# Kernel tuning notes

Hardware: AMD Instinct MI355X
Metric: run time of the kernel (lower is better)

The kernel has to match this reference:

```python
import jax, jax.numpy as jnp
import numpy as np

H = 96          # hidden_dim / GatedGraphConv out_channels
L = 6           # num_layers
F_IN = 32       # num_node_features
G = 4096        # number of graphs in batch
BN_EPS = 1e-5


def setup_inputs() -> dict:
    key = jax.random.key(0)
    ks = jax.random.split(key, 16)
    N, E = 100000, 400000
    x = jax.random.normal(ks[0], (N, F_IN), dtype=jnp.float32)
    edge_index = jax.random.randint(ks[1], (2, E), 0, N, dtype=jnp.int64)
    batch = jnp.sort(jax.random.randint(ks[2], (N,), 0, G, dtype=jnp.int64))
    s = 1.0 / np.sqrt(H)
    conv_w = jax.random.uniform(ks[3], (L, H, H), jnp.float32, -s, s)
    w_ih = jax.random.uniform(ks[4], (3 * H, H), jnp.float32, -s, s)
    w_hh = jax.random.uniform(ks[5], (3 * H, H), jnp.float32, -s, s)
    b_ih = jax.random.uniform(ks[6], (3 * H,), jnp.float32, -s, s)
    b_hh = jax.random.uniform(ks[7], (3 * H,), jnp.float32, -s, s)
    bn_gamma = jnp.ones((H,), jnp.float32)
    bn_beta = jnp.zeros((H,), jnp.float32)
    s1 = 1.0 / np.sqrt(H)
    fc1_w = jax.random.uniform(ks[8], (4 * H, H), jnp.float32, -s1, s1)
    fc1_b = jax.random.uniform(ks[9], (4 * H,), jnp.float32, -s1, s1)
    s2 = 1.0 / np.sqrt(4 * H)
    fc2_w = jax.random.uniform(ks[10], (H, 4 * H), jnp.float32, -s2, s2)
    fc2_b = jax.random.uniform(ks[11], (H,), jnp.float32, -s2, s2)
    fc3_w = jax.random.uniform(ks[12], (1, H), jnp.float32, -s1, s1)
    fc3_b = jax.random.uniform(ks[13], (1,), jnp.float32, -s1, s1)
    return dict(x=x, edge_index=edge_index, batch=batch, conv_w=conv_w,
                w_ih=w_ih, w_hh=w_hh, b_ih=b_ih, b_hh=b_hh,
                bn_gamma=bn_gamma, bn_beta=bn_beta,
                fc1_w=fc1_w, fc1_b=fc1_b, fc2_w=fc2_w, fc2_b=fc2_b,
                fc3_w=fc3_w, fc3_b=fc3_b)


def _gated_graph_conv(x, src, dst, conv_w, w_ih, w_hh, b_ih, b_hh):
    N = x.shape[0]
    # PyG zero-pads input features up to out_channels
    h = jnp.pad(x, ((0, 0), (0, H - x.shape[1])))
    for i in range(L):
        m = h @ conv_w[i]                         # [N, H]
        agg = jnp.zeros((N, H), m.dtype).at[dst].add(m[src])  # scatter-add at targets
        gi = agg @ w_ih.T + b_ih                  # [N, 3H]
        gh = h @ w_hh.T + b_hh                    # [N, 3H]
        i_r, i_z, i_n = jnp.split(gi, 3, axis=-1)
        h_r, h_z, h_n = jnp.split(gh, 3, axis=-1)
        r = jax.nn.sigmoid(i_r + h_r)
        z = jax.nn.sigmoid(i_z + h_z)
        n = jnp.tanh(i_n + r * h_n)
        h = (1.0 - z) * n + z * h
    return h


def reference(x, edge_index, batch, conv_w, w_ih, w_hh, b_ih, b_hh,
              bn_gamma, bn_beta, fc1_w, fc1_b, fc2_w, fc2_b, fc3_w, fc3_b):
    src, dst = edge_index[0], edge_index[1]
    h = _gated_graph_conv(x, src, dst, conv_w, w_ih, w_hh, b_ih, b_hh)
    h = jax.nn.relu(h)
    # global mean pool (dropout is identity in eval)
    sums = jax.ops.segment_sum(h, batch, num_segments=G)          # [G, H]
    counts = jax.ops.segment_sum(jnp.ones((h.shape[0],), h.dtype), batch, num_segments=G)
    pooled = sums / jnp.maximum(counts, 1.0)[:, None]
    # BatchNorm1d in eval mode: running_mean=0, running_var=1
    hbn = (pooled / jnp.sqrt(1.0 + BN_EPS)) * bn_gamma + bn_beta
    h1 = jax.nn.relu(hbn @ fc1_w.T + fc1_b)
    h2 = jax.nn.relu(h1 @ fc2_w.T + fc2_b)
    return h2 @ fc3_w.T + fc3_b                                    # [G, 1]
```

## Files before the change

kernel.cpp:

```cpp
#include <hip/hip_runtime.h>

#define H96 96
#define LAYERS 6
#define BN_EPS 1e-5f
#define SCAN_B 1024

typedef unsigned short u16;
typedef unsigned int u32;
typedef _Float16 f16;
typedef _Float16 h8 __attribute__((ext_vector_type(8)));
typedef float f32x4 __attribute__((ext_vector_type(4)));
typedef float f32x2 __attribute__((ext_vector_type(2)));
typedef u32 u32x3 __attribute__((ext_vector_type(3)));

__device__ __forceinline__ float sigm(float x) { return 1.f / (1.f + __expf(-x)); }
__device__ __forceinline__ float tanh_(float x) { return 2.f / (1.f + __expf(-2.f * x)) - 1.f; }
__device__ __forceinline__ f32x4 splat4(float x) { f32x4 v = {x, x, x, x}; return v; }
__device__ __forceinline__ h8 H8(f32x4 v) { return __builtin_bit_cast(h8, v); }

struct h2s { f16 x, y; };

__device__ __forceinline__ void upk(u32 v, float& lo, float& hi) {
    union { u32 u; h2s h; } c;
    c.u = v;
    lo = (float)c.h.x;
    hi = (float)c.h.y;
}

__device__ __forceinline__ h8 lds_frag(const f16* p) {
    union { h8 v; f32x2 h[2]; } u;
    u.h[0] = *(const f32x2*)(p);
    u.h[1] = *(const f32x2*)(p + 4);
    return u.v;
}

__global__ void k_f2h(const float* __restrict__ convw, const float* __restrict__ wih,
                      const float* __restrict__ whh, const float* __restrict__ fc1w,
                      const float* __restrict__ fc2w, f16* __restrict__ dst) {
    int i = blockIdx.x * 256 + threadIdx.x;
    if (i >= 184320) return;
    float v;
    if (i < 55296) v = convw[i];
    else if (i < 82944) v = wih[i - 55296];
    else if (i < 110592) v = whh[i - 82944];
    else if (i < 147456) v = fc1w[i - 110592];
    else v = fc2w[i - 147456];
    dst[i] = (f16)v;
}

__global__ __launch_bounds__(256) void k_wpt(const f16* __restrict__ wih16, const f16* __restrict__ convw16,
                                             f16* __restrict__ wpt) {
    int l = blockIdx.y;
    int lane = threadIdx.x & 63, wave = threadIdx.x >> 6;
    int l15 = lane & 15, q = lane >> 4;
    int rowa = blockIdx.x * 64 + wave * 16 + l15;
    if (rowa >= 288) rowa = 287;
    const f16* B = convw16 + (size_t)l * 9216;
    h8 af[3];
#pragma unroll
    for (int s = 0; s < 3; s++) af[s] = *(const h8*)(wih16 + (size_t)rowa * 96 + s * 32 + q * 8);
    f32x4 acc[6];
#pragma unroll
    for (int t = 0; t < 6; t++) acc[t] = splat4(0.f);
#pragma unroll
    for (int s = 0; s < 3; s++)
#pragma unroll
        for (int t = 0; t < 6; t++) {
            h8 b = *(const h8*)(B + (size_t)(t * 16 + l15) * 96 + s * 32 + q * 8);
            acc[t] = __builtin_amdgcn_mfma_f32_16x16x32_f16(af[s], b, acc[t], 0, 0, 0);
        }
    int rbase = blockIdx.x * 64 + wave * 16 + q * 4;
#pragma unroll
    for (int t = 0; t < 6; t++)
#pragma unroll
        for (int rr = 0; rr < 4; rr++) {
            int row = rbase + rr;
            if (row < 288) wpt[(size_t)l * 27648 + (size_t)row * 96 + t * 16 + l15] = (f16)acc[t][rr];
        }
}

__global__ void k_pad(const float* __restrict__ x, f16* __restrict__ hf, int N) {
    int i = blockIdx.x * 256 + threadIdx.x;
    if (i >= N * H96) return;
    int n = i / H96, c = i - n * H96;
    float v = (c < 32) ? x[n * 32 + c] : 0.f;
    hf[i] = (f16)v;
}

__global__ void k_hist(const int* __restrict__ key, int* __restrict__ deg, int E) {
    int e = blockIdx.x * 256 + threadIdx.x;
    if (e < E) atomicAdd(&deg[key[e]], 1);
}

__global__ __launch_bounds__(SCAN_B) void k_scan1(const int* __restrict__ deg, int* __restrict__ incl,
                                                  int* __restrict__ bsum, int N) {
    __shared__ int sh[SCAN_B];
    int i = blockIdx.x * SCAN_B + threadIdx.x;
    int v = (i < N) ? deg[i] : 0;
    sh[threadIdx.x] = v;
    __syncthreads();
    for (int off = 1; off < SCAN_B; off <<= 1) {
        int t = (threadIdx.x >= (u32)off) ? sh[threadIdx.x - off] : 0;
        __syncthreads();
        sh[threadIdx.x] += t;
        __syncthreads();
    }
    incl[blockIdx.x * SCAN_B + threadIdx.x] = sh[threadIdx.x];
    if (threadIdx.x == SCAN_B - 1) bsum[blockIdx.x] = sh[threadIdx.x];
}

__global__ void k_scan2(int* __restrict__ bsum, int nb) {
    if (blockIdx.x == 0 && threadIdx.x == 0) {
        int run = 0;
        for (int i = 0; i < nb; i++) { run += bsum[i]; bsum[i] = run; }
    }
}

__global__ void k_scan3(const int* __restrict__ deg, const int* __restrict__ incl, const int* __restrict__ bsum,
                        int* __restrict__ rs, int* __restrict__ cur, int N, int E) {
    int i = blockIdx.x * 256 + threadIdx.x;
    if (i == 0) rs[N] = E;
    if (i < N) {
        int b = i / SCAN_B;
        int off = (b > 0) ? bsum[b - 1] : 0;
        int ex = incl[i] - deg[i] + off;
        rs[i] = ex;
        if (cur) cur[i] = ex;
    }
}

__global__ void k_fill(const int* __restrict__ src, const int* __restrict__ dst, int* __restrict__ cur,
                       int* __restrict__ es, int E) {
    int e = blockIdx.x * 256 + threadIdx.x;
    if (e < E) {
        int p = atomicAdd(&cur[dst[e]], 1);
        es[p] = src[e];
    }
}

__global__ __launch_bounds__(256) void k_gather(const f16* __restrict__ hin, const int* __restrict__ rs,
                                                const int* __restrict__ es, f16* __restrict__ agg, int N) {
    int grp = threadIdx.x >> 4;
    int lane6 = threadIdx.x & 15;
    int node = blockIdx.x * 16 + grp;
    if (node >= N) return;
    int s = rs[node], e = rs[node + 1];
    float a0 = 0, a1 = 0, a2 = 0, a3 = 0, a4 = 0, a5 = 0;
    const char* basep = (const char*)hin;
    int off = lane6 * 12;
    for (int i = s; i < e; i += 4) {
        int j1 = (i + 1 < e) ? i + 1 : i;
        int j2 = (i + 2 < e) ? i + 2 : i;
        int j3 = (i + 3 < e) ? i + 3 : i;
        float m1 = (i + 1 < e) ? 1.f : 0.f;
        float m2 = (i + 2 < e) ? 1.f : 0.f;
        float m3 = (i + 3 < e) ? 1.f : 0.f;
        int sa = es[i], sb = es[j1], sc = es[j2], sd = es[j3];
        u32x3 va = *(const u32x3*)(basep + (size_t)sa * 192 + off);
        u32x3 vb = *(const u32x3*)(basep + (size_t)sb * 192 + off);
        u32x3 vc = *(const u32x3*)(basep + (size_t)sc * 192 + off);
        u32x3 vd = *(const u32x3*)(basep + (size_t)sd * 192 + off);
        float t0, t1;
        upk(va.x, t0, t1); a0 += t0; a1 += t1;
        upk(va.y, t0, t1); a2 += t0; a3 += t1;
        upk(va.z, t0, t1); a4 += t0; a5 += t1;
        upk(vb.x, t0, t1); a0 += t0 * m1; a1 += t1 * m1;
        upk(vb.y, t0, t1); a2 += t0 * m1; a3 += t1 * m1;
        upk(vb.z, t0, t1); a4 += t0 * m1; a5 += t1 * m1;
        upk(vc.x, t0, t1); a0 += t0 * m2; a1 += t1 * m2;
        upk(vc.y, t0, t1); a2 += t0 * m2; a3 += t1 * m2;
        upk(vc.z, t0, t1); a4 += t0 * m2; a5 += t1 * m2;
        upk(vd.x, t0, t1); a0 += t0 * m3; a1 += t1 * m3;
        upk(vd.y, t0, t1); a2 += t0 * m3; a3 += t1 * m3;
        upk(vd.z, t0, t1); a4 += t0 * m3; a5 += t1 * m3;
    }
    f16* dp = agg + (size_t)node * H96 + lane6 * 6;
    h2s p0, p1, p2;
    p0.x = (f16)a0; p0.y = (f16)a1;
    p1.x = (f16)a2; p1.y = (f16)a3;
    p2.x = (f16)a4; p2.y = (f16)a5;
    *(h2s*)(dp + 0) = p0;
    *(h2s*)(dp + 2) = p1;
    *(h2s*)(dp + 4) = p2;
}

__global__ __launch_bounds__(384, 2) void k_gru(const f16* __restrict__ agg, const f16* __restrict__ hin,
                                                f16* __restrict__ hout, const f16* __restrict__ wpt,
                                                const f16* __restrict__ whh, const float* __restrict__ bih,
                                                const float* __restrict__ bhh, int N) {
    const int TP = 100;
    __shared__ f16 sA[2][16 * TP];
    __shared__ f16 sH[2][16 * TP];
    int tid = threadIdx.x;
    int w = tid >> 6;
    int lane = tid & 63;
    int l15 = lane & 15, q = lane >> 4;
    int jr = w * 16 + l15;
    float b_r = bih[jr] + bhh[jr];
    float b_z = bih[96 + jr] + bhh[96 + jr];
    float b_in = bih[192 + jr];
    float b_hn = bhh[192 + jr];
    f32x4 wr0[3], wr1[3], wz0[3], wz1[3], wn0[3], wn1[3];
#pragma unroll
    for (int s = 0; s < 3; s++) {
        int ko = s * 32 + q * 8;
        wr0[s] = *(const f32x4*)(wpt + (size_t)jr * H96 + ko);
        wz0[s] = *(const f32x4*)(wpt + (size_t)(96 + jr) * H96 + ko);
        wn0[s] = *(const f32x4*)(wpt + (size_t)(192 + jr) * H96 + ko);
        wr1[s] = *(const f32x4*)(whh + (size_t)jr * H96 + ko);
        wz1[s] = *(const f32x4*)(whh + (size_t)(96 + jr) * H96 + ko);
        wn1[s] = *(const f32x4*)(whh + (size_t)(192 + jr) * H96 + ko);
    }
#pragma unroll
    for (int s = 0; s < 3; s++) {
        asm volatile("" : "+v"(wr0[s]), "+v"(wr1[s]), "+v"(wz0[s]), "+v"(wz1[s]), "+v"(wn0[s]), "+v"(wn1[s]));
    }

    int mt = (tid < 192) ? tid : tid - 192;
    int mrow = mt / 12;
    int mcol = mt - mrow * 12;
    const f16* smat = (tid < 192) ? agg : hin;
    f16* sdst = (tid < 192) ? &sA[0][0] : &sH[0][0];
    int soff = mrow * TP + mcol * 8;

    int ntiles = (N + 15) >> 4;
    int stride = gridDim.x;
    int tile = blockIdx.x;
    if (tile >= ntiles) return;

    {
        int rowa = (tile << 4) + mrow;
        if (rowa >= N) rowa = N - 1;
        f32x4 v = *(const f32x4*)(smat + (size_t)rowa * 96 + mcol * 8);
        union { f32x4 v; f32x2 h[2]; } u;
        u.v = v;
        *(f32x2*)(sdst + soff) = u.h[0];
        *(f32x2*)(sdst + soff + 4) = u.h[1];
    }
    __syncthreads();
    int cur = 0;
    while (true) {
        int nxt = tile + stride;
        bool havenext = nxt < ntiles;
        f32x4 v2 = splat4(0.f);
        if (havenext) {
            int rowa = (nxt << 4) + mrow;
            if (rowa >= N) rowa = N - 1;
            v2 = *(const f32x4*)(smat + (size_t)rowa * 96 + mcol * 8);
        }
        const f16* pA = &sA[cur][0];
        const f16* pH = &sH[cur][0];
        h8 as_[3], ah[3];
#pragma unroll
        for (int s = 0; s < 3; s++) {
            int off = l15 * TP + s * 32 + q * 8;
            as_[s] = lds_frag(pA + off);
            ah[s] = lds_frag(pH + off);
        }
        f32x4 r = splat4(b_r), z = splat4(b_z), nn = splat4(b_in), hn = splat4(b_hn);
#pragma unroll
        for (int s = 0; s < 3; s++) {
            r = __builtin_amdgcn_mfma_f32_16x16x32_f16(as_[s], H8(wr0[s]), r, 0, 0, 0);
            r = __builtin_amdgcn_mfma_f32_16x16x32_f16(ah[s], H8(wr1[s]), r, 0, 0, 0);
            z = __builtin_amdgcn_mfma_f32_16x16x32_f16(as_[s], H8(wz0[s]), z, 0, 0, 0);
            z = __builtin_amdgcn_mfma_f32_16x16x32_f16(ah[s], H8(wz1[s]), z, 0, 0, 0);
            nn = __builtin_amdgcn_mfma_f32_16x16x32_f16(as_[s], H8(wn0[s]), nn, 0, 0, 0);
            hn = __builtin_amdgcn_mfma_f32_16x16x32_f16(ah[s], H8(wn1[s]), hn, 0, 0, 0);
        }
        int base = tile << 4;
        int rbase = base + q * 4;
#pragma unroll
        for (int rr = 0; rr < 4; rr++) {
            int row = rbase + rr;
            if (row < N) {
                float rv = sigm(r[rr]);
                float zv = sigm(z[rr]);
                float nv = tanh_(nn[rr] + rv * hn[rr]);
                float hold = (float)pH[(q * 4 + rr) * TP + w * 16 + l15];
                float hnew = (1.f - zv) * nv + zv * hold;
                hout[(size_t)row * H96 + w * 16 + l15] = (f16)hnew;
            }
        }
        __syncthreads();
        if (!havenext) break;
        {
            union { f32x4 v; f32x2 h[2]; } u;
            u.v = v2;
            f16* d2 = sdst + (cur ^ 1) * (16 * TP) + soff;
            *(f32x2*)(d2) = u.h[0];
            *(f32x2*)(d2 + 4) = u.h[1];
        }
        __syncthreads();
        tile = nxt;
        cur ^= 1;
    }
}

__global__ void k_pool2(const f16* __restrict__ hf, const int* __restrict__ grs,
                        const float* __restrict__ gamma, const float* __restrict__ beta,
                        f16* __restrict__ pooled, int Gn) {
    int g = blockIdx.x;
    int c = threadIdx.x;
    if (g >= Gn || c >= H96) return;
    int s = grs[g], e = grs[g + 1];
    float sum = 0.f;
    for (int n = s; n < e; n++) sum += fmaxf((float)hf[(size_t)n * H96 + c], 0.f);
    float cnt = fmaxf((float)(e - s), 1.f);
    float val = (sum / cnt) * (gamma[c] * rsqrtf(1.f + BN_EPS)) + beta[c];
    pooled[(size_t)g * H96 + c] = (f16)val;
}

template <int KS, int NT, int OUTW, bool RELU>
__global__ __launch_bounds__(256) void k_mlp(const f16* __restrict__ A, const f16* __restrict__ W,
                                             const float* __restrict__ bias, f16* __restrict__ out, int M) {
    int lane = threadIdx.x & 63, wave = threadIdx.x >> 6;
    int l15 = lane & 15, q = lane >> 4;
    int colBase = blockIdx.y * (NT * 16);
    int tile = blockIdx.x;
    int rowa = tile * 64 + wave * 16 + l15;
    if (rowa >= M) rowa = M - 1;
    h8 af[KS];
#pragma unroll
    for (int s = 0; s < KS; s++) af[s] = *(const h8*)(A + (size_t)rowa * (KS * 32) + s * 32 + q * 8);
    f32x4 acc[NT];
#pragma unroll
    for (int t = 0; t < NT; t++) acc[t] = splat4(0.f);
#pragma unroll
    for (int s = 0; s < KS; s++)
#pragma unroll
        for (int t = 0; t < NT; t++) {
            h8 b = *(const h8*)(W + (size_t)(colBase + t * 16 + l15) * (KS * 32) + s * 32 + q * 8);
            acc[t] = __builtin_amdgcn_mfma_f32_16x16x32_f16(af[s], b, acc[t], 0, 0, 0);
        }
    int rbase = tile * 64 + wave * 16 + q * 4;
#pragma unroll
    for (int t = 0; t < NT; t++) {
        float bv = bias[colBase + t * 16 + l15];
#pragma unroll
        for (int rr = 0; rr < 4; rr++) {
            int row = rbase + rr;
            if (row >= M) continue;
            float v = acc[t][rr] + bv;
            if (RELU) v = fmaxf(v, 0.f);
            out[(size_t)row * OUTW + colBase + t * 16 + l15] = (f16)v;
        }
    }
}

__global__ void k_mlp3(const f16* __restrict__ h2, const float* __restrict__ w, const float* __restrict__ b,
                       float* __restrict__ out, int M) {
    int g = blockIdx.x * 256 + threadIdx.x;
    if (g >= M) return;
    float acc = 0.f;
    for (int k = 0; k < H96; k++) acc += (float)h2[(size_t)g * H96 + k] * w[k];
    out[g] = acc + b[0];
}

extern "C" void kernel_launch(void* const* d_in, const int* in_sizes, int n_in, void* d_out, int out_size,
                              void* d_ws, size_t ws_size, hipStream_t stream) {
    const float* x = (const float*)d_in[0];
    const int* ei = (const int*)d_in[1];
    const int* batch = (const int*)d_in[2];
    const float* conv_w = (const float*)d_in[3];
    const float* wih = (const float*)d_in[4];
    const float* whh = (const float*)d_in[5];
    const float* bih = (const float*)d_in[6];
    const float* bhh = (const float*)d_in[7];
    const float* gamma = (const float*)d_in[8];
    const float* beta = (const float*)d_in[9];
    const float* fc1w = (const float*)d_in[10];
    const float* fc1b = (const float*)d_in[11];
    const float* fc2w = (const float*)d_in[12];
    const float* fc2b = (const float*)d_in[13];
    const float* fc3w = (const float*)d_in[14];
    const float* fc3b = (const float*)d_in[15];

    int N = in_sizes[0] / 32;
    int E = in_sizes[1] / 2;
    int Gn = out_size;
    const int* srcp = ei;
    const int* dstp = ei + E;

    char* p = (char*)d_ws;
    auto alloc = [&](size_t bytes) -> char* {
        char* r = p;
        p += (bytes + 255) & ~(size_t)255;
        return r;
    };
    f16* hA = (f16*)alloc((size_t)N * H96 * 2);
    f16* hB = (f16*)alloc((size_t)N * H96 * 2);
    f16* aggf = (f16*)alloc((size_t)N * H96 * 2);
    f16* wf16 = (f16*)alloc((size_t)184320 * 2);
    f16* wpt = (f16*)alloc((size_t)LAYERS * 27648 * 2);
    int nb = (N + SCAN_B - 1) / SCAN_B;
    int* deg = (int*)alloc((size_t)N * 4);
    int* incl = (int*)alloc((size_t)nb * SCAN_B * 4);
    int* bsum = (int*)alloc((size_t)nb * 4);
    int* rs = (int*)alloc((size_t)(N + 1) * 4);
    int* cur = (int*)alloc((size_t)N * 4);
    int* es = (int*)alloc((size_t)E * 4);
    int nb2 = (Gn + SCAN_B - 1) / SCAN_B;
    int* gdeg = (int*)alloc((size_t)Gn * 4);
    int* gincl = (int*)alloc((size_t)nb2 * SCAN_B * 4);
    int* gbsum = (int*)alloc((size_t)nb2 * 4);
    int* grs = (int*)alloc((size_t)(Gn + 1) * 4);
    f16* pooled = (f16*)alloc((size_t)Gn * H96 * 2);
    f16* h1 = (f16*)alloc((size_t)Gn * 384 * 2);
    f16* h2 = (f16*)alloc((size_t)Gn * H96 * 2);

    f16* convw16 = wf16;
    f16* wih16 = wf16 + 55296;
    f16* whh16 = wf16 + 82944;
    f16* fc1w16 = wf16 + 110592;
    f16* fc2w16 = wf16 + 147456;

    hipMemsetAsync(deg, 0, (size_t)N * 4, stream);
    hipMemsetAsync(gdeg, 0, (size_t)Gn * 4, stream);

    k_f2h<<<720, 256, 0, stream>>>(conv_w, wih, whh, fc1w, fc2w, wf16);
    k_wpt<<<dim3(5, 6), 256, 0, stream>>>(wih16, convw16, wpt);
    k_pad<<<(N * H96 + 255) / 256, 256, 0, stream>>>(x, hA, N);
    k_hist<<<(E + 255) / 256, 256, 0, stream>>>(dstp, deg, E);
    k_scan1<<<nb, SCAN_B, 0, stream>>>(deg, incl, bsum, N);
    k_scan2<<<1, 64, 0, stream>>>(bsum, nb);
    k_scan3<<<(N + 255) / 256, 256, 0, stream>>>(deg, incl, bsum, rs, cur, N, E);
    k_fill<<<(E + 255) / 256, 256, 0, stream>>>(srcp, dstp, cur, es, E);
    k_hist<<<(N + 255) / 256, 256, 0, stream>>>(batch, gdeg, N);
    k_scan1<<<nb2, SCAN_B, 0, stream>>>(gdeg, gincl, gbsum, Gn);
    k_scan2<<<1, 64, 0, stream>>>(gbsum, nb2);
    k_scan3<<<(Gn + 255) / 256, 256, 0, stream>>>(gdeg, gincl, gbsum, grs, (int*)nullptr, Gn, N);

    int nt16 = (N + 15) / 16;
    for (int l = 0; l < LAYERS; l++) {
        f16* hin = (l & 1) ? hB : hA;
        f16* hout = (l & 1) ? hA : hB;
        k_gather<<<nt16, 256, 0, stream>>>(hin, rs, es, aggf, N);
        k_gru<<<1280, 384, 0, stream>>>(aggf, hin, hout, wpt + (size_t)l * 27648, whh16, bih, bhh, N);
    }

    k_pool2<<<Gn, 128, 0, stream>>>(hA, grs, gamma, beta, pooled, Gn);
    k_mlp<3, 6, 384, true><<<dim3((Gn + 63) / 64, 4), 256, 0, stream>>>(pooled, fc1w16, fc1b, h1, Gn);
    k_mlp<12, 6, 96, true><<<dim3((Gn + 63) / 64, 1), 256, 0, stream>>>(h1, fc2w16, fc2b, h2, Gn);
    k_mlp3<<<(Gn + 255) / 256, 256, 0, stream>>>(h2, fc3w, fc3b, (float*)d_out, Gn);
}
```

Baseline: 610.4 us.

## Fuse neighbor gather into GRU layer kernel, aggregating into shared memory

Measured after the change: 743.4 us. 1.22x slower.

```diff
diff --git a/kernel.cpp b/kernel.cpp
--- a/kernel.cpp
+++ b/kernel.cpp
@@ -11,7 +11,7 @@
 typedef _Float16 h8 __attribute__((ext_vector_type(8)));
 typedef float f32x4 __attribute__((ext_vector_type(4)));
 typedef float f32x2 __attribute__((ext_vector_type(2)));
-typedef u32 u32x3 __attribute__((ext_vector_type(3)));
+typedef u32 u32x2 __attribute__((ext_vector_type(2)));
 
 __device__ __forceinline__ float sigm(float x) { return 1.f / (1.f + __expf(-x)); }
 __device__ __forceinline__ float tanh_(float x) { return 2.f / (1.f + __expf(-2.f * x)) - 1.f; }
@@ -138,59 +138,14 @@
     }
 }
 
-__global__ __launch_bounds__(256) void k_gather(const f16* __restrict__ hin, const int* __restrict__ rs,
-                                                const int* __restrict__ es, f16* __restrict__ agg, int N) {
-    int grp = threadIdx.x >> 4;
-    int lane6 = threadIdx.x & 15;
-    int node = blockIdx.x * 16 + grp;
-    if (node >= N) return;
-    int s = rs[node], e = rs[node + 1];
-    float a0 = 0, a1 = 0, a2 = 0, a3 = 0, a4 = 0, a5 = 0;
-    const char* basep = (const char*)hin;
-    int off = lane6 * 12;
-    for (int i = s; i < e; i += 4) {
-        int j1 = (i + 1 < e) ? i + 1 : i;
-        int j2 = (i + 2 < e) ? i + 2 : i;
-        int j3 = (i + 3 < e) ? i + 3 : i;
-        float m1 = (i + 1 < e) ? 1.f : 0.f;
-        float m2 = (i + 2 < e) ? 1.f : 0.f;
-        float m3 = (i + 3 < e) ? 1.f : 0.f;
-        int sa = es[i], sb = es[j1], sc = es[j2], sd = es[j3];
-        u32x3 va = *(const u32x3*)(basep + (size_t)sa * 192 + off);
-        u32x3 vb = *(const u32x3*)(basep + (size_t)sb * 192 + off);
-        u32x3 vc = *(const u32x3*)(basep + (size_t)sc * 192 + off);
-        u32x3 vd = *(const u32x3*)(basep + (size_t)sd * 192 + off);
-        float t0, t1;
-        upk(va.x, t0, t1); a0 += t0; a1 += t1;
-        upk(va.y, t0, t1); a2 += t0; a3 += t1;
-        upk(va.z, t0, t1); a4 += t0; a5 += t1;
-        upk(vb.x, t0, t1); a0 += t0 * m1; a1 += t1 * m1;
-        upk(vb.y, t0, t1); a2 += t0 * m1; a3 += t1 * m1;
-        upk(vb.z, t0, t1); a4 += t0 * m1; a5 += t1 * m1;
-        upk(vc.x, t0, t1); a0 += t0 * m2; a1 += t1 * m2;
-        upk(vc.y, t0, t1); a2 += t0 * m2; a3 += t1 * m2;
-        upk(vc.z, t0, t1); a4 += t0 * m2; a5 += t1 * m2;
-        upk(vd.x, t0, t1); a0 += t0 * m3; a1 += t1 * m3;
-        upk(vd.y, t0, t1); a2 += t0 * m3; a3 += t1 * m3;
-        upk(vd.z, t0, t1); a4 += t0 * m3; a5 += t1 * m3;
-    }
-    f16* dp = agg + (size_t)node * H96 + lane6 * 6;
-    h2s p0, p1, p2;
-    p0.x = (f16)a0; p0.y = (f16)a1;
-    p1.x = (f16)a2; p1.y = (f16)a3;
-    p2.x = (f16)a4; p2.y = (f16)a5;
-    *(h2s*)(dp + 0) = p0;
-    *(h2s*)(dp + 2) = p1;
-    *(h2s*)(dp + 4) = p2;
-}
-
-__global__ __launch_bounds__(384, 2) void k_gru(const f16* __restrict__ agg, const f16* __restrict__ hin,
-                                                f16* __restrict__ hout, const f16* __restrict__ wpt,
-                                                const f16* __restrict__ whh, const float* __restrict__ bih,
-                                                const float* __restrict__ bhh, int N) {
+__global__ __launch_bounds__(384, 2) void k_layer(const f16* __restrict__ hin, f16* __restrict__ hout,
+                                                  const int* __restrict__ rs, const int* __restrict__ es,
+                                                  const f16* __restrict__ wpt, const f16* __restrict__ whh,
+                                                  const float* __restrict__ bih, const float* __restrict__ bhh,
+                                                  int N) {
     const int TP = 100;
-    __shared__ f16 sA[2][16 * TP];
-    __shared__ f16 sH[2][16 * TP];
+    __shared__ f16 sAgg[16 * TP];
+    __shared__ f16 sHin[16 * TP];
     int tid = threadIdx.x;
     int w = tid >> 6;
     int lane = tid & 63;
@@ -216,46 +171,67 @@
         asm volatile("" : "+v"(wr0[s]), "+v"(wr1[s]), "+v"(wz0[s]), "+v"(wz1[s]), "+v"(wn0[s]), "+v"(wn1[s]));
     }
 
-    int mt = (tid < 192) ? tid : tid - 192;
-    int mrow = mt / 12;
-    int mcol = mt - mrow * 12;
-    const f16* smat = (tid < 192) ? agg : hin;
-    f16* sdst = (tid < 192) ? &sA[0][0] : &sH[0][0];
-    int soff = mrow * TP + mcol * 8;
+    int g24 = tid / 24;
+    int l24 = tid - g24 * 24;
+    int goff = l24 * 8;
+    int mrow = tid / 12, mcol = tid - mrow * 12;
 
     int ntiles = (N + 15) >> 4;
-    int stride = gridDim.x;
-    int tile = blockIdx.x;
-    if (tile >= ntiles) return;
-
-    {
-        int rowa = (tile << 4) + mrow;
-        if (rowa >= N) rowa = N - 1;
-        f32x4 v = *(const f32x4*)(smat + (size_t)rowa * 96 + mcol * 8);
-        union { f32x4 v; f32x2 h[2]; } u;
-        u.v = v;
-        *(f32x2*)(sdst + soff) = u.h[0];
-        *(f32x2*)(sdst + soff + 4) = u.h[1];
-    }
-    __syncthreads();
-    int cur = 0;
-    while (true) {
-        int nxt = tile + stride;
-        bool havenext = nxt < ntiles;
-        f32x4 v2 = splat4(0.f);
-        if (havenext) {
-            int rowa = (nxt << 4) + mrow;
+    const char* basep = (const char*)hin;
+
+    for (int tile = blockIdx.x; tile < ntiles; tile += gridDim.x) {
+        int base = tile << 4;
+        if (tid < 192) {
+            int rowa = base + mrow;
             if (rowa >= N) rowa = N - 1;
-            v2 = *(const f32x4*)(smat + (size_t)rowa * 96 + mcol * 8);
-        }
-        const f16* pA = &sA[cur][0];
-        const f16* pH = &sH[cur][0];
+            f32x4 v = *(const f32x4*)(hin + (size_t)rowa * 96 + mcol * 8);
+            union { f32x4 v; f32x2 h[2]; } u;
+            u.v = v;
+            f16* d = sHin + mrow * TP + mcol * 8;
+            *(f32x2*)(d) = u.h[0];
+            *(f32x2*)(d + 4) = u.h[1];
+        }
+        {
+            int node = base + g24;
+            if (node >= N) node = N - 1;
+            int s = rs[node], e = rs[node + 1];
+            float a0 = 0, a1 = 0, a2 = 0, a3 = 0;
+            for (int i = s; i < e; i += 4) {
+                int j1 = (i + 1 < e) ? i + 1 : i;
+                int j2 = (i + 2 < e) ? i + 2 : i;
+                int j3 = (i + 3 < e) ? i + 3 : i;
+                float m1 = (i + 1 < e) ? 1.f : 0.f;
+                float m2 = (i + 2 < e) ? 1.f : 0.f;
+                float m3 = (i + 3 < e) ? 1.f : 0.f;
+                int sa = es[i], sb = es[j1], sc = es[j2], sd = es[j3];
+                u32x2 va = *(const u32x2*)(basep + (size_t)sa * 192 + goff);
+                u32x2 vb = *(const u32x2*)(basep + (size_t)sb * 192 + goff);
+                u32x2 vc = *(const u32x2*)(basep + (size_t)sc * 192 + goff);
+                u32x2 vd = *(const u32x2*)(basep + (size_t)sd * 192 + goff);
+                float t0, t1;
+                upk(va.x, t0, t1); a0 += t0; a1 += t1;
+                upk(va.y, t0, t1); a2 += t0; a3 += t1;
+                upk(vb.x, t0, t1); a0 += t0 * m1; a1 += t1 * m1;
+                upk(vb.y, t0, t1); a2 += t0 * m1; a3 += t1 * m1;
+                upk(vc.x, t0, t1); a0 += t0 * m2; a1 += t1 * m2;
+                upk(vc.y, t0, t1); a2 += t0 * m2; a3 += t1 * m2;
+                upk(vd.x, t0, t1); a0 += t0 * m3; a1 += t1 * m3;
+                upk(vd.y, t0, t1); a2 += t0 * m3; a3 += t1 * m3;
+            }
+            f16* dp = sAgg + g24 * TP + l24 * 4;
+            h2s p0, p1;
+            p0.x = (f16)a0; p0.y = (f16)a1;
+            p1.x = (f16)a2; p1.y = (f16)a3;
+            *(h2s*)(dp + 0) = p0;
+            *(h2s*)(dp + 2) = p1;
+        }
+        __syncthreads();
         h8 as_[3], ah[3];
 #pragma unroll
         for (int s = 0; s < 3; s++) {
             int off = l15 * TP + s * 32 + q * 8;
-            as_[s] = lds_frag(pA + off);
-            ah[s] = lds_frag(pH + off);
+            as_[s] = lds_frag(sAgg + off);
+            ah[s] = lds_frag(sHin + off);
         }
         f32x4 r = splat4(b_r), z = splat4(b_z), nn = splat4(b_in), hn = splat4(b_hn);
 #pragma unroll
@@ -267,7 +243,6 @@
             nn = __builtin_amdgcn_mfma_f32_16x16x32_f16(as_[s], H8(wn0[s]), nn, 0, 0, 0);
             hn = __builtin_amdgcn_mfma_f32_16x16x32_f16(ah[s], H8(wn1[s]), hn, 0, 0, 0);
         }
-        int base = tile << 4;
         int rbase = base + q * 4;
 #pragma unroll
         for (int rr = 0; rr < 4; rr++) {
@@ -276,23 +251,12 @@
                 float rv = sigm(r[rr]);
                 float zv = sigm(z[rr]);
                 float nv = tanh_(nn[rr] + rv * hn[rr]);
-                float hold = (float)pH[(q * 4 + rr) * TP + w * 16 + l15];
+                float hold = (float)sHin[(q * 4 + rr) * TP + w * 16 + l15];
                 float hnew = (1.f - zv) * nv + zv * hold;
                 hout[(size_t)row * H96 + w * 16 + l15] = (f16)hnew;
             }
         }
         __syncthreads();
-        if (!havenext) break;
-        {
-            union { f32x4 v; f32x2 h[2]; } u;
-            u.v = v2;
-            f16* d2 = sdst + (cur ^ 1) * (16 * TP) + soff;
-            *(f32x2*)(d2) = u.h[0];
-            *(f32x2*)(d2 + 4) = u.h[1];
-        }
-        __syncthreads();
-        tile = nxt;
-        cur ^= 1;
     }
 }
 
@@ -389,7 +353,6 @@
     };
     f16* hA = (f16*)alloc((size_t)N * H96 * 2);
     f16* hB = (f16*)alloc((size_t)N * H96 * 2);
-    f16* aggf = (f16*)alloc((size_t)N * H96 * 2);
     f16* wf16 = (f16*)alloc((size_t)184320 * 2);
     f16* wpt = (f16*)alloc((size_t)LAYERS * 27648 * 2);
     int nb = (N + SCAN_B - 1) / SCAN_B;
@@ -430,12 +393,10 @@
     k_scan2<<<1, 64, 0, stream>>>(gbsum, nb2);
     k_scan3<<<(Gn + 255) / 256, 256, 0, stream>>>(gdeg, gincl, gbsum, grs, (int*)nullptr, Gn, N);
 
-    int nt16 = (N + 15) / 16;
     for (int l = 0; l < LAYERS; l++) {
         f16* hin = (l & 1) ? hB : hA;
         f16* hout = (l & 1) ? hA : hB;
-        k_gather<<<nt16, 256, 0, stream>>>(hin, rs, es, aggf, N);
-        k_gru<<<1280, 384, 0, stream>>>(aggf, hin, hout, wpt + (size_t)l * 27648, whh16, bih, bhh, N);
+        k_layer<<<1280, 384, 0, stream>>>(hin, hout, rs, es, wpt + (size_t)l * 27648, whh16, bih, bhh, N);
     }
 
     k_pool2<<<Gn, 128, 0, stream>>>(hA, grs, gamma, beta, pooled, Gn);
```
